# Kernel optimization log

Hardware: AMD Instinct MI355X
Metric: run time of the kernel (lower is better)

The kernel has to match this reference:

```python
import jax, jax.numpy as jnp
import numpy as np

IN_FEATURES = 4096
OUT_FEATURES = 12288
INT8_MAX = 127.0


def setup_inputs() -> dict:
    key = jax.random.key(0)
    kx, kw, ks, kb = jax.random.split(key, 4)
    x = jax.random.normal(kx, (8192, IN_FEATURES), dtype=jnp.float32)
    # pre-quantized int8 weight, stored [out_features, in_features] like the torch module
    weight = jax.random.randint(kw, (OUT_FEATURES, IN_FEATURES), -127, 128, dtype=jnp.int8)
    # per-output-channel weight scale, [out_features, 1]
    weight_scale = (jax.random.uniform(ks, (OUT_FEATURES, 1), dtype=jnp.float32) * 0.02 + 1e-4)
    bias = jax.random.normal(kb, (OUT_FEATURES,), dtype=jnp.float32) * 0.01
    return {"x": x, "weight": weight, "weight_scale": weight_scale, "bias": bias}


def _dynamic_int8_quant(x):
    # symmetric per-token quantization: scale = amax(|x|) / 127
    amax = jnp.max(jnp.abs(x), axis=-1, keepdims=True)  # [M, 1]
    scale = jnp.maximum(amax, 1e-8) / INT8_MAX
    x_q = jnp.clip(jnp.round(x / scale), -INT8_MAX, INT8_MAX).astype(jnp.int8)
    return x_q, scale


def reference(x, weight, weight_scale, bias):
    x_q, x_scale = _dynamic_int8_quant(x)                    # [M,K] int8, [M,1] f32
    # int8 GEMM with int32 accumulation: [M,K] @ [K,N]
    acc = jnp.matmul(x_q.astype(jnp.int32), weight.T.astype(jnp.int32))  # [M,N] int32
    # epilogue: dequant with per-token and per-channel scales, then bias add
    out = acc.astype(jnp.float32) * x_scale * weight_scale[:, 0][None, :] + bias[None, :]
    return out.astype(x.dtype)
```

## Files before the change

### kernel.cpp

```cpp
#include <hip/hip_runtime.h>
#include <stdint.h>

#define M_DIM 8192
#define K_DIM 4096
#define N_DIM 12288

typedef int v4i __attribute__((ext_vector_type(4)));

#define GLDS16(g, l)                                                         \
  __builtin_amdgcn_global_load_lds(                                          \
      (const __attribute__((address_space(1))) void*)(g),                    \
      (__attribute__((address_space(3))) void*)(l), 16, 0, 0)

#define BARRIER() asm volatile("s_barrier" ::: "memory")
#define VMCNT4() asm volatile("s_waitcnt vmcnt(4)" ::: "memory")
#define VMCNT0() asm volatile("s_waitcnt vmcnt(0)" ::: "memory")

__global__ __launch_bounds__(256) void quant_rows(const float* __restrict__ x,
                                                  int8_t* __restrict__ xq,
                                                  float* __restrict__ xs) {
  const int row = blockIdx.x;
  const int t = threadIdx.x;
  const float* xr = x + (size_t)row * K_DIM;

  float4 v[4];
  float amax = 0.f;
#pragma unroll
  for (int i = 0; i < 4; ++i) {
    v[i] = reinterpret_cast<const float4*>(xr)[t * 4 + i];
    amax = fmaxf(amax, fmaxf(fmaxf(fabsf(v[i].x), fabsf(v[i].y)),
                             fmaxf(fabsf(v[i].z), fabsf(v[i].w))));
  }
#pragma unroll
  for (int off = 32; off > 0; off >>= 1)
    amax = fmaxf(amax, __shfl_xor(amax, off));

  __shared__ float smax[4];
  if ((t & 63) == 0) smax[t >> 6] = amax;
  __syncthreads();
  amax = fmaxf(fmaxf(smax[0], smax[1]), fmaxf(smax[2], smax[3]));

  const float scale = fmaxf(amax, 1e-8f) / 127.f;

  union {
    int8_t b[16];
    v4i v;
  } p;
  const float* pv = reinterpret_cast<const float*>(v);
#pragma unroll
  for (int i = 0; i < 16; ++i) {
    float r = rintf(pv[i] / scale);
    r = fminf(127.f, fmaxf(-127.f, r));
    p.b[i] = (int8_t)(int)r;
  }
  reinterpret_cast<v4i*>(xq + (size_t)row * K_DIM)[t] = p.v;
  if (t == 0) xs[row] = scale;
}

__global__ __launch_bounds__(256) void pack_w(const int* __restrict__ w32,
                                              int8_t* __restrict__ w8) {
  const size_t i = ((size_t)blockIdx.x * 256 + threadIdx.x) * 16;
  const int4* src = reinterpret_cast<const int4*>(w32 + i);
  union {
    int8_t b[16];
    v4i v;
  } p;
#pragma unroll
  for (int c = 0; c < 4; ++c) {
    int4 q = src[c];
    p.b[c * 4 + 0] = (int8_t)q.x;
    p.b[c * 4 + 1] = (int8_t)q.y;
    p.b[c * 4 + 2] = (int8_t)q.z;
    p.b[c * 4 + 3] = (int8_t)q.w;
  }
  *reinterpret_cast<v4i*>(w8 + i) = p.v;
}

#define BM 256
#define BN 256
#define BKB 128
#define NTILES (K_DIM / BKB)

__global__ __launch_bounds__(512, 2) void gemm_i8(
    const int8_t* __restrict__ xq, const float* __restrict__ xs,
    const int8_t* __restrict__ w8, const float* __restrict__ wsc,
    const float* __restrict__ bias, float* __restrict__ out) {
  __shared__ __align__(16) int8_t lds[131072];
  const v4i* Lv = (const v4i*)lds;

  const int t = threadIdx.x;
  const int lane = t & 63;
  const int w = t >> 6;
  const int wr = w >> 2;
  const int wc = w & 3;
  const int fr = lane & 15;
  const int kq = lane >> 4;
  const int l7 = lane & 7;

  const int NT_N = N_DIM / BN;
  const int nwg = (M_DIM / BM) * NT_N;
  int bid = (int)blockIdx.x;
  bid = (bid & 7) * (nwg >> 3) + (bid >> 3);
  const int rowBase = (bid / NT_N) * BM;
  const int colBase = (bid % NT_N) * BN;

  const int srow = t >> 3;
  const int gslot = (t & 7) ^ (srow & 7);
  const int8_t* gA = xq + (size_t)(rowBase + srow) * K_DIM + gslot * 16;
  const int8_t* gB = w8 + (size_t)(colBase + srow) * K_DIM + gslot * 16;
  int8_t* ldsw = lds + w * 1024;

#define STAGE_A(c, r0, k0) \
  GLDS16(gA + (size_t)(r0) * K_DIM + (k0), ldsw + (c) * 32768 + (r0) * 128)
#define STAGE_B(c, r0, k0) \
  GLDS16(gB + (size_t)(r0) * K_DIM + (k0), ldsw + 65536 + (c) * 32768 + (r0) * 128)

  const int s0_ = kq ^ l7;
  const int s1_ = s0_ ^ 4;
  const int rA = wr * 128 + fr;
  const int rB = wc * 64 + fr;

#define LA(c, mh, mi, ks) \
  Lv[((c) << 11) + ((rA + (mh) * 64 + (mi) * 16) << 3) + ((ks) ? s1_ : s0_)]
#define LB(c, ni, ks) \
  Lv[4096 + ((c) << 11) + ((rB + (ni) * 16) << 3) + ((ks) ? s1_ : s0_)]

  v4i acc[8][4];
#pragma unroll
  for (int i = 0; i < 8; ++i)
#pragma unroll
    for (int j = 0; j < 4; ++j) acc[i][j] = (v4i){0, 0, 0, 0};

  STAGE_A(0, 0, 0); STAGE_A(0, 64, 0); STAGE_A(0, 128, 0); STAGE_A(0, 192, 0);
  STAGE_B(0, 0, 0); STAGE_B(0, 64, 0); STAGE_B(0, 128, 0); STAGE_B(0, 192, 0);
  STAGE_A(1, 0, BKB); STAGE_A(1, 64, BKB); STAGE_A(1, 128, BKB); STAGE_A(1, 192, BKB);
  VMCNT4();
  BARRIER();

  v4i af[4], bf[4];

#define PHASE(c, MH, KS, LOADB, ...)                                          \
  {                                                                           \
    _Pragma("unroll") for (int mi = 0; mi < 4; ++mi)                          \
        af[mi] = LA(c, MH, mi, KS);                                           \
    if (LOADB) {                                                              \
      _Pragma("unroll") for (int ni = 0; ni < 4; ++ni)                        \
          bf[ni] = LB(c, ni, KS);                                             \
    }                                                                         \
    __VA_ARGS__                                                               \
    BARRIER();                                                                \
    __builtin_amdgcn_s_setprio(1);                                            \
    _Pragma("unroll") for (int ni = 0; ni < 4; ++ni)                          \
        _Pragma("unroll") for (int mi = 0; mi < 4; ++mi)                      \
            acc[(MH) * 4 + mi][ni] = __builtin_amdgcn_mfma_i32_16x16x64_i8(   \
                af[mi], bf[ni], acc[(MH) * 4 + mi][ni], 0, 0, 0);             \
    __builtin_amdgcn_s_setprio(0);                                            \
    BARRIER();                                                                \
  }

  for (int tt = 0; tt < NTILES - 2; ++tt) {
    const int c = tt & 1;
    const int k1 = (tt + 1) * BKB;
    const int k2 = (tt + 2) * BKB;
    PHASE(c, 0, 0, 1, STAGE_B(c ^ 1, 0, k1); STAGE_B(c ^ 1, 64, k1);)
    PHASE(c, 1, 0, 0, STAGE_B(c ^ 1, 128, k1); STAGE_B(c ^ 1, 192, k1);)
    PHASE(c, 0, 1, 1, )
    PHASE(c, 1, 1, 0, )
    STAGE_A(c, 0, k2); STAGE_A(c, 64, k2); STAGE_A(c, 128, k2); STAGE_A(c, 192, k2);
    VMCNT4();
    BARRIER();
  }
  {
    const int k1 = (NTILES - 1) * BKB;
    PHASE(0, 0, 0, 1, STAGE_B(1, 0, k1); STAGE_B(1, 64, k1);)
    PHASE(0, 1, 0, 0, STAGE_B(1, 128, k1); STAGE_B(1, 192, k1);)
    PHASE(0, 0, 1, 1, )
    PHASE(0, 1, 1, 0, )
    VMCNT0();
    BARRIER();
  }
  {
    PHASE(1, 0, 0, 1, )
    PHASE(1, 1, 0, 0, )
    PHASE(1, 0, 1, 1, )
    PHASE(1, 1, 1, 0, )
  }

  const int orow0 = rowBase + wr * 128;
  const int ocol0 = colBase + wc * 64;
  const int rsub = kq * 4;
#pragma unroll
  for (int mi8 = 0; mi8 < 8; ++mi8) {
    const int r0 = orow0 + mi8 * 16 + rsub;
    float s4[4];
#pragma unroll
    for (int r = 0; r < 4; ++r) s4[r] = xs[r0 + r];
#pragma unroll
    for (int ni = 0; ni < 4; ++ni) {
      const int col = ocol0 + ni * 16 + fr;
      const float wf = wsc[col];
      const float bb = bias[col];
#pragma unroll
      for (int r = 0; r < 4; ++r)
        out[(size_t)(r0 + r) * N_DIM + col] =
            (float)acc[mi8][ni][r] * s4[r] * wf + bb;
    }
  }
}

extern "C" void kernel_launch(void* const* d_in, const int* in_sizes, int n_in,
                              void* d_out, int out_size, void* d_ws,
                              size_t ws_size, hipStream_t stream) {
  const float* x = (const float*)d_in[0];
  const int* w32 = (const int*)d_in[1];
  const float* wscale = (const float*)d_in[2];
  const float* bias = (const float*)d_in[3];
  float* out = (float*)d_out;

  int8_t* xq = (int8_t*)d_ws;
  float* xs = (float*)((char*)d_ws + (size_t)M_DIM * K_DIM);
  int8_t* w8 = (int8_t*)((char*)d_ws + (size_t)M_DIM * K_DIM + M_DIM * 4);

  quant_rows<<<M_DIM, 256, 0, stream>>>(x, xq, xs);
  pack_w<<<(N_DIM * K_DIM) / (256 * 16), 256, 0, stream>>>(w32, w8);
  gemm_i8<<<(M_DIM / BM) * (N_DIM / BN), 512, 0, stream>>>(xq, xs, w8, wscale,
                                                           bias, out);
}
```

Measured before the change: 506.1 us.

## Switch GEMM to 32x32x32 int8 MFMA and fuse quant/pack prep kernels

```diff
diff --git a/kernel.cpp b/kernel.cpp
--- a/kernel.cpp
+++ b/kernel.cpp
@@ -6,6 +6,7 @@
 #define N_DIM 12288
 
 typedef int v4i __attribute__((ext_vector_type(4)));
+typedef int v16i __attribute__((ext_vector_type(16)));
 
 #define GLDS16(g, l)                                                         \
   __builtin_amdgcn_global_load_lds(                                          \
@@ -16,64 +17,65 @@
 #define VMCNT4() asm volatile("s_waitcnt vmcnt(4)" ::: "memory")
 #define VMCNT0() asm volatile("s_waitcnt vmcnt(0)" ::: "memory")
 
-__global__ __launch_bounds__(256) void quant_rows(const float* __restrict__ x,
-                                                  int8_t* __restrict__ xq,
-                                                  float* __restrict__ xs) {
-  const int row = blockIdx.x;
+__global__ __launch_bounds__(256) void prep(const float* __restrict__ x,
+                                            int8_t* __restrict__ xq,
+                                            float* __restrict__ xs,
+                                            const int* __restrict__ w32,
+                                            int8_t* __restrict__ w8) {
   const int t = threadIdx.x;
-  const float* xr = x + (size_t)row * K_DIM;
-
-  float4 v[4];
-  float amax = 0.f;
-#pragma unroll
-  for (int i = 0; i < 4; ++i) {
-    v[i] = reinterpret_cast<const float4*>(xr)[t * 4 + i];
-    amax = fmaxf(amax, fmaxf(fmaxf(fabsf(v[i].x), fabsf(v[i].y)),
-                             fmaxf(fabsf(v[i].z), fabsf(v[i].w))));
-  }
-#pragma unroll
-  for (int off = 32; off > 0; off >>= 1)
-    amax = fmaxf(amax, __shfl_xor(amax, off));
-
-  __shared__ float smax[4];
-  if ((t & 63) == 0) smax[t >> 6] = amax;
-  __syncthreads();
-  amax = fmaxf(fmaxf(smax[0], smax[1]), fmaxf(smax[2], smax[3]));
-
-  const float scale = fmaxf(amax, 1e-8f) / 127.f;
-
-  union {
-    int8_t b[16];
-    v4i v;
-  } p;
-  const float* pv = reinterpret_cast<const float*>(v);
-#pragma unroll
-  for (int i = 0; i < 16; ++i) {
-    float r = rintf(pv[i] / scale);
-    r = fminf(127.f, fmaxf(-127.f, r));
-    p.b[i] = (int8_t)(int)r;
-  }
-  reinterpret_cast<v4i*>(xq + (size_t)row * K_DIM)[t] = p.v;
-  if (t == 0) xs[row] = scale;
-}
-
-__global__ __launch_bounds__(256) void pack_w(const int* __restrict__ w32,
-                                              int8_t* __restrict__ w8) {
-  const size_t i = ((size_t)blockIdx.x * 256 + threadIdx.x) * 16;
-  const int4* src = reinterpret_cast<const int4*>(w32 + i);
-  union {
-    int8_t b[16];
-    v4i v;
-  } p;
-#pragma unroll
-  for (int c = 0; c < 4; ++c) {
-    int4 q = src[c];
-    p.b[c * 4 + 0] = (int8_t)q.x;
-    p.b[c * 4 + 1] = (int8_t)q.y;
-    p.b[c * 4 + 2] = (int8_t)q.z;
-    p.b[c * 4 + 3] = (int8_t)q.w;
-  }
-  *reinterpret_cast<v4i*>(w8 + i) = p.v;
+  if ((int)blockIdx.x < M_DIM) {
+    const int row = blockIdx.x;
+    const float* xr = x + (size_t)row * K_DIM;
+
+    float4 v[4];
+    float amax = 0.f;
+#pragma unroll
+    for (int i = 0; i < 4; ++i) {
+      v[i] = reinterpret_cast<const float4*>(xr)[t * 4 + i];
+      amax = fmaxf(amax, fmaxf(fmaxf(fabsf(v[i].x), fabsf(v[i].y)),
+                               fmaxf(fabsf(v[i].z), fabsf(v[i].w))));
+    }
+#pragma unroll
+    for (int off = 32; off > 0; off >>= 1)
+      amax = fmaxf(amax, __shfl_xor(amax, off));
+
+    __shared__ float smax[4];
+    if ((t & 63) == 0) smax[t >> 6] = amax;
+    __syncthreads();
+    amax = fmaxf(fmaxf(smax[0], smax[1]), fmaxf(smax[2], smax[3]));
+
+    const float scale = fmaxf(amax, 1e-8f) / 127.f;
+
+    union {
+      int8_t b[16];
+      v4i v;
+    } p;
+    const float* pv = reinterpret_cast<const float*>(v);
+#pragma unroll
+    for (int i = 0; i < 16; ++i) {
+      float r = rintf(pv[i] / scale);
+      r = fminf(127.f, fmaxf(-127.f, r));
+      p.b[i] = (int8_t)(int)r;
+    }
+    reinterpret_cast<v4i*>(xq + (size_t)row * K_DIM)[t] = p.v;
+    if (t == 0) xs[row] = scale;
+  } else {
+    const size_t i = (((size_t)blockIdx.x - M_DIM) * 256 + t) * 16;
+    const int4* src = reinterpret_cast<const int4*>(w32 + i);
+    union {
+      int8_t b[16];
+      v4i v;
+    } p;
+#pragma unroll
+    for (int c = 0; c < 4; ++c) {
+      int4 q = src[c];
+      p.b[c * 4 + 0] = (int8_t)q.x;
+      p.b[c * 4 + 1] = (int8_t)q.y;
+      p.b[c * 4 + 2] = (int8_t)q.z;
+      p.b[c * 4 + 3] = (int8_t)q.w;
+    }
+    *reinterpret_cast<v4i*>(w8 + i) = p.v;
+  }
 }
 
 #define BM 256
@@ -93,8 +95,8 @@
   const int w = t >> 6;
   const int wr = w >> 2;
   const int wc = w & 3;
-  const int fr = lane & 15;
-  const int kq = lane >> 4;
+  const int l31 = lane & 31;
+  const int hi = lane >> 5;
   const int l7 = lane & 7;
 
   const int NT_N = N_DIM / BN;
@@ -115,21 +117,25 @@
 #define STAGE_B(c, r0, k0) \
   GLDS16(gB + (size_t)(r0) * K_DIM + (k0), ldsw + 65536 + (c) * 32768 + (r0) * 128)
 
-  const int s0_ = kq ^ l7;
-  const int s1_ = s0_ ^ 4;
-  const int rA = wr * 128 + fr;
-  const int rB = wc * 64 + fr;
-
-#define LA(c, mh, mi, ks) \
-  Lv[((c) << 11) + ((rA + (mh) * 64 + (mi) * 16) << 3) + ((ks) ? s1_ : s0_)]
-#define LB(c, ni, ks) \
-  Lv[4096 + ((c) << 11) + ((rB + (ni) * 16) << 3) + ((ks) ? s1_ : s0_)]
-
-  v4i acc[8][4];
-#pragma unroll
-  for (int i = 0; i < 8; ++i)
-#pragma unroll
-    for (int j = 0; j < 4; ++j) acc[i][j] = (v4i){0, 0, 0, 0};
+  const int sl0 = (0 + hi) ^ l7;
+  const int sl1 = (2 + hi) ^ l7;
+  const int sl2 = (4 + hi) ^ l7;
+  const int sl3 = (6 + hi) ^ l7;
+  const int rAb = wr * 128 + l31;
+  const int rBb = wc * 64 + l31;
+
+#define LA(c, mh, mi, sl) \
+  Lv[((c) << 11) + ((rAb + (mh) * 64 + (mi) * 32) << 3) + (sl)]
+#define LB(c, ni, sl) \
+  Lv[4096 + ((c) << 11) + ((rBb + (ni) * 32) << 3) + (sl)]
+
+  v16i acc[4][2];
+#pragma unroll
+  for (int i = 0; i < 4; ++i)
+#pragma unroll
+    for (int j = 0; j < 2; ++j)
+#pragma unroll
+      for (int r = 0; r < 16; ++r) acc[i][j][r] = 0;
 
   STAGE_A(0, 0, 0); STAGE_A(0, 64, 0); STAGE_A(0, 128, 0); STAGE_A(0, 192, 0);
   STAGE_B(0, 0, 0); STAGE_B(0, 64, 0); STAGE_B(0, 128, 0); STAGE_B(0, 192, 0);
@@ -137,25 +143,32 @@
   VMCNT4();
   BARRIER();
 
-  v4i af[4], bf[4];
-
-#define PHASE(c, MH, KS, LOADB, ...)                                          \
-  {                                                                           \
-    _Pragma("unroll") for (int mi = 0; mi < 4; ++mi)                          \
-        af[mi] = LA(c, MH, mi, KS);                                           \
-    if (LOADB) {                                                              \
-      _Pragma("unroll") for (int ni = 0; ni < 4; ++ni)                        \
-          bf[ni] = LB(c, ni, KS);                                             \
-    }                                                                         \
-    __VA_ARGS__                                                               \
-    BARRIER();                                                                \
-    __builtin_amdgcn_s_setprio(1);                                            \
-    _Pragma("unroll") for (int ni = 0; ni < 4; ++ni)                          \
-        _Pragma("unroll") for (int mi = 0; mi < 4; ++mi)                      \
-            acc[(MH) * 4 + mi][ni] = __builtin_amdgcn_mfma_i32_16x16x64_i8(   \
-                af[mi], bf[ni], acc[(MH) * 4 + mi][ni], 0, 0, 0);             \
-    __builtin_amdgcn_s_setprio(0);                                            \
-    BARRIER();                                                                \
+  v4i af[2][2], bf[2][2];
+
+#define PHASE(c, MH, KS2, LOADB, ...)                                          \
+  {                                                                            \
+    af[0][0] = LA(c, MH, 0, (KS2) ? sl2 : sl0);                                \
+    af[0][1] = LA(c, MH, 0, (KS2) ? sl3 : sl1);                                \
+    af[1][0] = LA(c, MH, 1, (KS2) ? sl2 : sl0);                                \
+    af[1][1] = LA(c, MH, 1, (KS2) ? sl3 : sl1);                                \
+    if (LOADB) {                                                               \
+      bf[0][0] = LB(c, 0, (KS2) ? sl2 : sl0);                                  \
+      bf[0][1] = LB(c, 0, (KS2) ? sl3 : sl1);                                  \
+      bf[1][0] = LB(c, 1, (KS2) ? sl2 : sl0);                                  \
+      bf[1][1] = LB(c, 1, (KS2) ? sl3 : sl1);                                  \
+    }                                                                          \
+    __VA_ARGS__                                                                \
+    BARRIER();                                                                 \
+    __builtin_amdgcn_s_setprio(1);                                             \
+    _Pragma("unroll") for (int kk = 0; kk < 2; ++kk)                           \
+        _Pragma("unroll") for (int ni = 0; ni < 2; ++ni)                       \
+            _Pragma("unroll") for (int mi = 0; mi < 2; ++mi)                   \
+                acc[(MH) * 2 + mi][ni] =                                       \
+                    __builtin_amdgcn_mfma_i32_32x32x32_i8(                     \
+                        af[mi][kk], bf[ni][kk], acc[(MH) * 2 + mi][ni], 0, 0,  \
+                        0);                                                    \
+    __builtin_amdgcn_s_setprio(0);                                             \
+    BARRIER();                                                                 \
   }
 
   for (int tt = 0; tt < NTILES - 2; ++tt) {
@@ -188,22 +201,27 @@
 
   const int orow0 = rowBase + wr * 128;
   const int ocol0 = colBase + wc * 64;
-  const int rsub = kq * 4;
-#pragma unroll
-  for (int mi8 = 0; mi8 < 8; ++mi8) {
-    const int r0 = orow0 + mi8 * 16 + rsub;
-    float s4[4];
-#pragma unroll
-    for (int r = 0; r < 4; ++r) s4[r] = xs[r0 + r];
-#pragma unroll
-    for (int ni = 0; ni < 4; ++ni) {
-      const int col = ocol0 + ni * 16 + fr;
+#pragma unroll
+  for (int mi = 0; mi < 4; ++mi) {
+    const int rbase = orow0 + mi * 32 + hi * 4;
+    float sarr[16];
+#pragma unroll
+    for (int g = 0; g < 4; ++g)
+#pragma unroll
+      for (int r = 0; r < 4; ++r) sarr[g * 4 + r] = xs[rbase + g * 8 + r];
+#pragma unroll
+    for (int ni = 0; ni < 2; ++ni) {
+      const int col = ocol0 + ni * 32 + l31;
       const float wf = wsc[col];
       const float bb = bias[col];
 #pragma unroll
-      for (int r = 0; r < 4; ++r)
-        out[(size_t)(r0 + r) * N_DIM + col] =
-            (float)acc[mi8][ni][r] * s4[r] * wf + bb;
+      for (int g = 0; g < 4; ++g)
+#pragma unroll
+        for (int r = 0; r < 4; ++r) {
+          const int row = rbase + g * 8 + r;
+          out[(size_t)row * N_DIM + col] =
+              (float)acc[mi][ni][g * 4 + r] * sarr[g * 4 + r] * wf + bb;
+        }
     }
   }
 }
@@ -221,8 +239,8 @@
   float* xs = (float*)((char*)d_ws + (size_t)M_DIM * K_DIM);
   int8_t* w8 = (int8_t*)((char*)d_ws + (size_t)M_DIM * K_DIM + M_DIM * 4);
 
-  quant_rows<<<M_DIM, 256, 0, stream>>>(x, xq, xs);
-  pack_w<<<(N_DIM * K_DIM) / (256 * 16), 256, 0, stream>>>(w32, w8);
+  const int packBlocks = (N_DIM * K_DIM) / (256 * 16);
+  prep<<<M_DIM + packBlocks, 256, 0, stream>>>(x, xq, xs, w32, w8);
   gemm_i8<<<(M_DIM / BM) * (N_DIM / BN), 512, 0, stream>>>(xq, xs, w8, wscale,
                                                            bias, out);
 }
```

Result: slower. 548.8 us (+8.4%).

## Merge prep kernels and restructure GEMM prefetch to interleave A and B staging

Applied to the files above, without the earlier changes.

```diff
diff --git a/kernel.cpp b/kernel.cpp
--- a/kernel.cpp
+++ b/kernel.cpp
@@ -13,67 +13,68 @@
       (__attribute__((address_space(3))) void*)(l), 16, 0, 0)
 
 #define BARRIER() asm volatile("s_barrier" ::: "memory")
-#define VMCNT4() asm volatile("s_waitcnt vmcnt(4)" ::: "memory")
+#define VMCNT2() asm volatile("s_waitcnt vmcnt(2)" ::: "memory")
 #define VMCNT0() asm volatile("s_waitcnt vmcnt(0)" ::: "memory")
 
-__global__ __launch_bounds__(256) void quant_rows(const float* __restrict__ x,
-                                                  int8_t* __restrict__ xq,
-                                                  float* __restrict__ xs) {
-  const int row = blockIdx.x;
+__global__ __launch_bounds__(256) void prep(const float* __restrict__ x,
+                                            int8_t* __restrict__ xq,
+                                            float* __restrict__ xs,
+                                            const int* __restrict__ w32,
+                                            int8_t* __restrict__ w8) {
   const int t = threadIdx.x;
-  const float* xr = x + (size_t)row * K_DIM;
-
-  float4 v[4];
-  float amax = 0.f;
-#pragma unroll
-  for (int i = 0; i < 4; ++i) {
-    v[i] = reinterpret_cast<const float4*>(xr)[t * 4 + i];
-    amax = fmaxf(amax, fmaxf(fmaxf(fabsf(v[i].x), fabsf(v[i].y)),
-                             fmaxf(fabsf(v[i].z), fabsf(v[i].w))));
-  }
-#pragma unroll
-  for (int off = 32; off > 0; off >>= 1)
-    amax = fmaxf(amax, __shfl_xor(amax, off));
-
-  __shared__ float smax[4];
-  if ((t & 63) == 0) smax[t >> 6] = amax;
-  __syncthreads();
-  amax = fmaxf(fmaxf(smax[0], smax[1]), fmaxf(smax[2], smax[3]));
-
-  const float scale = fmaxf(amax, 1e-8f) / 127.f;
-
-  union {
-    int8_t b[16];
-    v4i v;
-  } p;
-  const float* pv = reinterpret_cast<const float*>(v);
-#pragma unroll
-  for (int i = 0; i < 16; ++i) {
-    float r = rintf(pv[i] / scale);
-    r = fminf(127.f, fmaxf(-127.f, r));
-    p.b[i] = (int8_t)(int)r;
-  }
-  reinterpret_cast<v4i*>(xq + (size_t)row * K_DIM)[t] = p.v;
-  if (t == 0) xs[row] = scale;
-}
-
-__global__ __launch_bounds__(256) void pack_w(const int* __restrict__ w32,
-                                              int8_t* __restrict__ w8) {
-  const size_t i = ((size_t)blockIdx.x * 256 + threadIdx.x) * 16;
-  const int4* src = reinterpret_cast<const int4*>(w32 + i);
-  union {
-    int8_t b[16];
-    v4i v;
-  } p;
-#pragma unroll
-  for (int c = 0; c < 4; ++c) {
-    int4 q = src[c];
-    p.b[c * 4 + 0] = (int8_t)q.x;
-    p.b[c * 4 + 1] = (int8_t)q.y;
-    p.b[c * 4 + 2] = (int8_t)q.z;
-    p.b[c * 4 + 3] = (int8_t)q.w;
-  }
-  *reinterpret_cast<v4i*>(w8 + i) = p.v;
+  if ((int)blockIdx.x < M_DIM) {
+    const int row = blockIdx.x;
+    const float* xr = x + (size_t)row * K_DIM;
+
+    float4 v[4];
+    float amax = 0.f;
+#pragma unroll
+    for (int i = 0; i < 4; ++i) {
+      v[i] = reinterpret_cast<const float4*>(xr)[t * 4 + i];
+      amax = fmaxf(amax, fmaxf(fmaxf(fabsf(v[i].x), fabsf(v[i].y)),
+                               fmaxf(fabsf(v[i].z), fabsf(v[i].w))));
+    }
+#pragma unroll
+    for (int off = 32; off > 0; off >>= 1)
+      amax = fmaxf(amax, __shfl_xor(amax, off));
+
+    __shared__ float smax[4];
+    if ((t & 63) == 0) smax[t >> 6] = amax;
+    __syncthreads();
+    amax = fmaxf(fmaxf(smax[0], smax[1]), fmaxf(smax[2], smax[3]));
+
+    const float scale = fmaxf(amax, 1e-8f) / 127.f;
+
+    union {
+      int8_t b[16];
+      v4i v;
+    } p;
+    const float* pv = reinterpret_cast<const float*>(v);
+#pragma unroll
+    for (int i = 0; i < 16; ++i) {
+      float r = rintf(pv[i] / scale);
+      r = fminf(127.f, fmaxf(-127.f, r));
+      p.b[i] = (int8_t)(int)r;
+    }
+    reinterpret_cast<v4i*>(xq + (size_t)row * K_DIM)[t] = p.v;
+    if (t == 0) xs[row] = scale;
+  } else {
+    const size_t i = (((size_t)blockIdx.x - M_DIM) * 256 + t) * 16;
+    const int4* src = reinterpret_cast<const int4*>(w32 + i);
+    union {
+      int8_t b[16];
+      v4i v;
+    } p;
+#pragma unroll
+    for (int c = 0; c < 4; ++c) {
+      int4 q = src[c];
+      p.b[c * 4 + 0] = (int8_t)q.x;
+      p.b[c * 4 + 1] = (int8_t)q.y;
+      p.b[c * 4 + 2] = (int8_t)q.z;
+      p.b[c * 4 + 3] = (int8_t)q.w;
+    }
+    *reinterpret_cast<v4i*>(w8 + i) = p.v;
+  }
 }
 
 #define BM 256
@@ -131,15 +132,14 @@
 #pragma unroll
     for (int j = 0; j < 4; ++j) acc[i][j] = (v4i){0, 0, 0, 0};
 
-  STAGE_A(0, 0, 0); STAGE_A(0, 64, 0); STAGE_A(0, 128, 0); STAGE_A(0, 192, 0);
   STAGE_B(0, 0, 0); STAGE_B(0, 64, 0); STAGE_B(0, 128, 0); STAGE_B(0, 192, 0);
-  STAGE_A(1, 0, BKB); STAGE_A(1, 64, BKB); STAGE_A(1, 128, BKB); STAGE_A(1, 192, BKB);
-  VMCNT4();
+  STAGE_A(0, 0, 0); STAGE_A(0, 128, 0); STAGE_A(0, 64, 0); STAGE_A(0, 192, 0);
+  VMCNT2();
   BARRIER();
 
   v4i af[4], bf[4];
 
-#define PHASE(c, MH, KS, LOADB, ...)                                          \
+#define PHASE(c, MH, KS, LOADB, STG, WAIT)                                    \
   {                                                                           \
     _Pragma("unroll") for (int mi = 0; mi < 4; ++mi)                          \
         af[mi] = LA(c, MH, mi, KS);                                           \
@@ -147,7 +147,7 @@
       _Pragma("unroll") for (int ni = 0; ni < 4; ++ni)                        \
           bf[ni] = LB(c, ni, KS);                                             \
     }                                                                         \
-    __VA_ARGS__                                                               \
+    STG;                                                                      \
     BARRIER();                                                                \
     __builtin_amdgcn_s_setprio(1);                                            \
     _Pragma("unroll") for (int ni = 0; ni < 4; ++ni)                          \
@@ -155,35 +155,24 @@
             acc[(MH) * 4 + mi][ni] = __builtin_amdgcn_mfma_i32_16x16x64_i8(   \
                 af[mi], bf[ni], acc[(MH) * 4 + mi][ni], 0, 0, 0);             \
     __builtin_amdgcn_s_setprio(0);                                            \
+    WAIT;                                                                     \
     BARRIER();                                                                \
   }
 
-  for (int tt = 0; tt < NTILES - 2; ++tt) {
+  for (int tt = 0; tt < NTILES - 1; ++tt) {
     const int c = tt & 1;
+    const int d = c ^ 1;
     const int k1 = (tt + 1) * BKB;
-    const int k2 = (tt + 2) * BKB;
-    PHASE(c, 0, 0, 1, STAGE_B(c ^ 1, 0, k1); STAGE_B(c ^ 1, 64, k1);)
-    PHASE(c, 1, 0, 0, STAGE_B(c ^ 1, 128, k1); STAGE_B(c ^ 1, 192, k1);)
-    PHASE(c, 0, 1, 1, )
-    PHASE(c, 1, 1, 0, )
-    STAGE_A(c, 0, k2); STAGE_A(c, 64, k2); STAGE_A(c, 128, k2); STAGE_A(c, 192, k2);
-    VMCNT4();
-    BARRIER();
+    PHASE(c, 0, 0, 1, { STAGE_B(d, 0, k1); STAGE_B(d, 64, k1); }, VMCNT2());
+    PHASE(c, 1, 0, 0, { STAGE_B(d, 128, k1); STAGE_B(d, 192, k1); }, );
+    PHASE(c, 0, 1, 1, { STAGE_A(d, 0, k1); STAGE_A(d, 128, k1); }, );
+    PHASE(c, 1, 1, 0, { STAGE_A(d, 64, k1); STAGE_A(d, 192, k1); }, VMCNT2());
   }
   {
-    const int k1 = (NTILES - 1) * BKB;
-    PHASE(0, 0, 0, 1, STAGE_B(1, 0, k1); STAGE_B(1, 64, k1);)
-    PHASE(0, 1, 0, 0, STAGE_B(1, 128, k1); STAGE_B(1, 192, k1);)
-    PHASE(0, 0, 1, 1, )
-    PHASE(0, 1, 1, 0, )
-    VMCNT0();
-    BARRIER();
-  }
-  {
-    PHASE(1, 0, 0, 1, )
-    PHASE(1, 1, 0, 0, )
-    PHASE(1, 0, 1, 1, )
-    PHASE(1, 1, 1, 0, )
+    PHASE(1, 0, 0, 1, , VMCNT0());
+    PHASE(1, 1, 0, 0, , );
+    PHASE(1, 0, 1, 1, , );
+    PHASE(1, 1, 1, 0, , );
   }
 
   const int orow0 = rowBase + wr * 128;
@@ -221,8 +210,8 @@
   float* xs = (float*)((char*)d_ws + (size_t)M_DIM * K_DIM);
   int8_t* w8 = (int8_t*)((char*)d_ws + (size_t)M_DIM * K_DIM + M_DIM * 4);
 
-  quant_rows<<<M_DIM, 256, 0, stream>>>(x, xq, xs);
-  pack_w<<<(N_DIM * K_DIM) / (256 * 16), 256, 0, stream>>>(w32, w8);
+  const int packBlocks = (N_DIM * K_DIM) / (256 * 16);
+  prep<<<M_DIM + packBlocks, 256, 0, stream>>>(x, xq, xs, w32, w8);
   gemm_i8<<<(M_DIM / BM) * (N_DIM / BN), 512, 0, stream>>>(xq, xs, w8, wscale,
                                                            bias, out);
 }
```

Result: no change. 503.5 us (-0.5%).
